# Kernel tuning notes

Hardware: AMD Instinct MI355X
Metric: run time of the kernel (lower is better)

The kernel has to match this reference:

```python
import jax, jax.numpy as jnp
import numpy as np

IGNORE_INDEX = 255
BOUNDARY_WEIGHT = 2.0


def setup_inputs() -> dict:
    key = jax.random.key(0)
    k1, k2 = jax.random.split(key)
    inputs = jax.random.normal(k1, (8, 21, 512, 512), dtype=jnp.float32)
    targets = jax.random.randint(k2, (8, 512, 512), 0, 21, dtype=jnp.int64)
    return {"inputs": inputs, "targets": targets}


def _boundary_map(targets):
    # Faithful to the original loops: for each interior (i, j), take the 3x3
    # patch over ALL batches; compute max-min over the ROW axis (dim=1) per
    # column; if ANY entry (across batch and the 3 columns) differs, mark
    # (i, j) as boundary for ALL batch elements.
    t = targets
    # row-wise (vertical) 3-tap max/min over rows i-1, i, i+1 -> (B, H-2, W)
    rmax = jnp.maximum(jnp.maximum(t[:, :-2, :], t[:, 1:-1, :]), t[:, 2:, :])
    rmin = jnp.minimum(jnp.minimum(t[:, :-2, :], t[:, 1:-1, :]), t[:, 2:, :])
    diff = (rmax - rmin) > 0  # (B, H-2, W)
    # any over the 3 patch columns j-1, j, j+1 -> (B, H-2, W-2)
    cany = diff[:, :, :-2] | diff[:, :, 1:-1] | diff[:, :, 2:]
    # any over batch (the original `.any()` reduces over everything)
    bmap = jnp.any(cany, axis=0)  # (H-2, W-2)
    boundary = jnp.zeros(t.shape, dtype=jnp.float32)
    boundary = boundary.at[:, 1:-1, 1:-1].set(
        jnp.broadcast_to(bmap.astype(jnp.float32), (t.shape[0],) + bmap.shape)
    )
    return boundary


def reference(inputs, targets):
    # per-pixel cross entropy with ignore_index (reduction='none' -> 0 at ignored)
    logp = jax.nn.log_softmax(inputs, axis=1)  # (B, C, H, W)
    valid = targets != IGNORE_INDEX
    safe_t = jnp.where(valid, targets, 0)
    ce = -jnp.take_along_axis(logp, safe_t[:, None, :, :], axis=1)[:, 0]  # (B,H,W)
    ce = jnp.where(valid, ce, 0.0)
    boundary = _boundary_map(targets)
    weighted = ce * (1.0 + BOUNDARY_WEIGHT * boundary)
    return weighted.mean()
```

## Files before the change

kernel.cpp:

```cpp
#include <hip/hip_runtime.h>

#define BATCH 8
#define NCLS 21
#define H 512
#define W 512
#define IGNORE_INDEX 255
#define HW (H * W)
#define NPIX (BATCH * HW)
#define NBLK 2048

typedef float vfloat4 __attribute__((ext_vector_type(4)));

__global__ __launch_bounds__(256)
void fused_kernel(const float* __restrict__ x, const int* __restrict__ t,
                  float* __restrict__ partial) {
    int tid = blockIdx.x * blockDim.x + threadIdx.x;
    int idx4 = tid << 2;
    int b = idx4 >> 18;
    int hw = idx4 & (HW - 1);
    int h = hw >> 9;
    int w = hw & (W - 1);

    unsigned bd0 = 0, bd1 = 0, bd2 = 0, bd3 = 0;
    if (h > 0 && h < H - 1) {
        int offL = (w == 0) ? 0 : -1;
        int offR = (w == W - 4) ? 3 : 4;
        #pragma unroll 1
        for (int bb = 0; bb < BATCH; ++bb) {
            const int* rm = t + bb * HW + h * W + w;
            const int* ra = rm - W;
            const int* rz = rm + W;
            int4 a4 = *(const int4*)ra;
            int4 m4 = *(const int4*)rm;
            int4 z4 = *(const int4*)rz;
            int aL = ra[offL], mL = rm[offL], zL = rz[offL];
            int aR = ra[offR], mR = rm[offR], zR = rz[offR];
            unsigned cdL = (unsigned)((aL != mL) | (mL != zL));
            unsigned cd0 = (unsigned)((a4.x != m4.x) | (m4.x != z4.x));
            unsigned cd1 = (unsigned)((a4.y != m4.y) | (m4.y != z4.y));
            unsigned cd2 = (unsigned)((a4.z != m4.z) | (m4.z != z4.z));
            unsigned cd3 = (unsigned)((a4.w != m4.w) | (m4.w != z4.w));
            unsigned cdR = (unsigned)((aR != mR) | (mR != zR));
            bd0 |= cdL | cd0 | cd1;
            bd1 |= cd0 | cd1 | cd2;
            bd2 |= cd1 | cd2 | cd3;
            bd3 |= cd2 | cd3 | cdR;
            if (bd0 & bd1 & bd2 & bd3) break;
        }
        if (w == 0) bd0 = 0;
        if (w == W - 4) bd3 = 0;
    }

    int4 tg = *(const int4*)(t + idx4);
    bool va0 = (tg.x != IGNORE_INDEX), va1 = (tg.y != IGNORE_INDEX);
    bool va2 = (tg.z != IGNORE_INDEX), va3 = (tg.w != IGNORE_INDEX);
    int st0 = va0 ? tg.x : 0, st1 = va1 ? tg.y : 0;
    int st2 = va2 ? tg.z : 0, st3 = va3 ? tg.w : 0;

    const float* p = x + (size_t)b * NCLS * HW + hw;
    float s0 = 0.f, s1 = 0.f, s2 = 0.f, s3 = 0.f;
    float xt0 = 0.f, xt1 = 0.f, xt2 = 0.f, xt3 = 0.f;
    #pragma unroll
    for (int c = 0; c < NCLS; ++c) {
        vfloat4 q = *(const vfloat4*)(p + (size_t)c * HW);
        s0 += __expf(q.x); if (c == st0) xt0 = q.x;
        s1 += __expf(q.y); if (c == st1) xt1 = q.y;
        s2 += __expf(q.z); if (c == st2) xt2 = q.z;
        s3 += __expf(q.w); if (c == st3) xt3 = q.w;
    }

    float ce0 = va0 ? (__logf(s0) - xt0) : 0.f;
    float ce1 = va1 ? (__logf(s1) - xt1) : 0.f;
    float ce2 = va2 ? (__logf(s2) - xt2) : 0.f;
    float ce3 = va3 ? (__logf(s3) - xt3) : 0.f;

    float local = ce0 * (1.f + 2.f * (float)bd0) + ce1 * (1.f + 2.f * (float)bd1) +
                  ce2 * (1.f + 2.f * (float)bd2) + ce3 * (1.f + 2.f * (float)bd3);

    #pragma unroll
    for (int off = 32; off > 0; off >>= 1)
        local += __shfl_down(local, off, 64);

    __shared__ float smem[4];
    int lane = threadIdx.x & 63;
    int wave = threadIdx.x >> 6;
    if (lane == 0) smem[wave] = local;
    __syncthreads();
    if (threadIdx.x == 0)
        partial[blockIdx.x] = smem[0] + smem[1] + smem[2] + smem[3];
}

__global__ void reduce_kernel(const float* __restrict__ partial,
                              float* __restrict__ out) {
    float s = 0.0f;
    for (int i = threadIdx.x; i < NBLK; i += 256) s += partial[i];
    #pragma unroll
    for (int off = 32; off > 0; off >>= 1)
        s += __shfl_down(s, off, 64);
    __shared__ float smem[4];
    int lane = threadIdx.x & 63;
    int wave = threadIdx.x >> 6;
    if (lane == 0) smem[wave] = s;
    __syncthreads();
    if (threadIdx.x == 0)
        out[0] = (smem[0] + smem[1] + smem[2] + smem[3]) * (1.0f / (float)NPIX);
}

extern "C" void kernel_launch(void* const* d_in, const int* in_sizes, int n_in,
                              void* d_out, int out_size, void* d_ws, size_t ws_size,
                              hipStream_t stream) {
    const float* x = (const float*)d_in[0];
    const int* t = (const int*)d_in[1];
    float* out = (float*)d_out;
    float* partial = (float*)d_ws;

    fused_kernel<<<NBLK, 256, 0, stream>>>(x, t, partial);
    reduce_kernel<<<1, 256, 0, stream>>>(partial, out);
}
```

Baseline: 248.9 us.

## Process two rows per thread with nontemporal prefetched logit loads

Each thread now handles 8 pixels, 4 columns in each of two rows two apart, so the grid is halved. Logit loads use nontemporal hints and are software-prefetched one class ahead. The boundary computation is moved into a helper that returns a bitmask. The intent is more memory-level parallelism per thread and less cache pollution from the streamed logits, at the cost of more registers per thread and fewer waves in flight.

```diff
diff --git a/kernel.cpp b/kernel.cpp
--- a/kernel.cpp
+++ b/kernel.cpp
@@ -7,21 +7,13 @@
 #define IGNORE_INDEX 255
 #define HW (H * W)
 #define NPIX (BATCH * HW)
-#define NBLK 2048
+#define NBLK 1024
 
 typedef float vfloat4 __attribute__((ext_vector_type(4)));
 
-__global__ __launch_bounds__(256)
-void fused_kernel(const float* __restrict__ x, const int* __restrict__ t,
-                  float* __restrict__ partial) {
-    int tid = blockIdx.x * blockDim.x + threadIdx.x;
-    int idx4 = tid << 2;
-    int b = idx4 >> 18;
-    int hw = idx4 & (HW - 1);
-    int h = hw >> 9;
-    int w = hw & (W - 1);
-
-    unsigned bd0 = 0, bd1 = 0, bd2 = 0, bd3 = 0;
+__device__ __forceinline__ unsigned boundary4(const int* __restrict__ t,
+                                              int h, int w) {
+    unsigned r = 0;
     if (h > 0 && h < H - 1) {
         int offL = (w == 0) ? 0 : -1;
         int offR = (w == W - 4) ? 3 : 4;
@@ -41,41 +33,81 @@
             unsigned cd2 = (unsigned)((a4.z != m4.z) | (m4.z != z4.z));
             unsigned cd3 = (unsigned)((a4.w != m4.w) | (m4.w != z4.w));
             unsigned cdR = (unsigned)((aR != mR) | (mR != zR));
-            bd0 |= cdL | cd0 | cd1;
-            bd1 |= cd0 | cd1 | cd2;
-            bd2 |= cd1 | cd2 | cd3;
-            bd3 |= cd2 | cd3 | cdR;
-            if (bd0 & bd1 & bd2 & bd3) break;
+            r |= (cdL | cd0 | cd1) | ((cd0 | cd1 | cd2) << 1) |
+                 ((cd1 | cd2 | cd3) << 2) | ((cd2 | cd3 | cdR) << 3);
+            if (r == 0xFu) break;
         }
-        if (w == 0) bd0 = 0;
-        if (w == W - 4) bd3 = 0;
+        if (w == 0) r &= ~1u;
+        if (w == W - 4) r &= ~8u;
+    }
+    return r;
+}
+
+__global__ __launch_bounds__(256)
+void fused_kernel(const float* __restrict__ x, const int* __restrict__ t,
+                  float* __restrict__ partial) {
+    int blk = blockIdx.x;
+    int b = blk >> 7;
+    int hq = blk & 127;
+    int i = threadIdx.x;
+    int h0 = (hq << 2) + (i >> 7);
+    int w = (i & 127) << 2;
+
+    int hw0 = (h0 << 9) + w;
+    int hw1 = hw0 + 2 * W;
+
+    unsigned bdA = boundary4(t, h0, w);
+    unsigned bdB = boundary4(t, h0 + 2, w);
+    int4 tgA = *(const int4*)(t + b * HW + hw0);
+    int4 tgB = *(const int4*)(t + b * HW + hw1);
+
+    bool vA0 = tgA.x != IGNORE_INDEX, vA1 = tgA.y != IGNORE_INDEX;
+    bool vA2 = tgA.z != IGNORE_INDEX, vA3 = tgA.w != IGNORE_INDEX;
+    bool vB0 = tgB.x != IGNORE_INDEX, vB1 = tgB.y != IGNORE_INDEX;
+    bool vB2 = tgB.z != IGNORE_INDEX, vB3 = tgB.w != IGNORE_INDEX;
+    int sA0 = vA0 ? tgA.x : 0, sA1 = vA1 ? tgA.y : 0;
+    int sA2 = vA2 ? tgA.z : 0, sA3 = vA3 ? tgA.w : 0;
+    int sB0 = vB0 ? tgB.x : 0, sB1 = vB1 ? tgB.y : 0;
+    int sB2 = vB2 ? tgB.z : 0, sB3 = vB3 ? tgB.w : 0;
+
+    const float* p0 = x + (size_t)b * NCLS * HW + hw0;
+    const float* p1 = x + (size_t)b * NCLS * HW + hw1;
+
+    vfloat4 a0 = __builtin_nontemporal_load((const vfloat4*)p0);
+    vfloat4 a1 = __builtin_nontemporal_load((const vfloat4*)p1);
+
+    float eA0 = 0.f, eA1 = 0.f, eA2 = 0.f, eA3 = 0.f;
+    float eB0 = 0.f, eB1 = 0.f, eB2 = 0.f, eB3 = 0.f;
+    float xA0 = 0.f, xA1 = 0.f, xA2 = 0.f, xA3 = 0.f;
+    float xB0 = 0.f, xB1 = 0.f, xB2 = 0.f, xB3 = 0.f;
+
+    #pragma unroll
+    for (int c = 0; c < NCLS; ++c) {
+        vfloat4 n0, n1;
+        if (c + 1 < NCLS) {
+            n0 = __builtin_nontemporal_load((const vfloat4*)(p0 + (size_t)(c + 1) * HW));
+            n1 = __builtin_nontemporal_load((const vfloat4*)(p1 + (size_t)(c + 1) * HW));
+        }
+        eA0 += __expf(a0.x); if (c == sA0) xA0 = a0.x;
+        eA1 += __expf(a0.y); if (c == sA1) xA1 = a0.y;
+        eA2 += __expf(a0.z); if (c == sA2) xA2 = a0.z;
+        eA3 += __expf(a0.w); if (c == sA3) xA3 = a0.w;
+        eB0 += __expf(a1.x); if (c == sB0) xB0 = a1.x;
+        eB1 += __expf(a1.y); if (c == sB1) xB1 = a1.y;
+        eB2 += __expf(a1.z); if (c == sB2) xB2 = a1.z;
+        eB3 += __expf(a1.w); if (c == sB3) xB3 = a1.w;
+        a0 = n0; a1 = n1;
     }
 
-    int4 tg = *(const int4*)(t + idx4);
-    bool va0 = (tg.x != IGNORE_INDEX), va1 = (tg.y != IGNORE_INDEX);
-    bool va2 = (tg.z != IGNORE_INDEX), va3 = (tg.w != IGNORE_INDEX);
-    int st0 = va0 ? tg.x : 0, st1 = va1 ? tg.y : 0;
-    int st2 = va2 ? tg.z : 0, st3 = va3 ? tg.w : 0;
-
-    const float* p = x + (size_t)b * NCLS * HW + hw;
-    float s0 = 0.f, s1 = 0.f, s2 = 0.f, s3 = 0.f;
-    float xt0 = 0.f, xt1 = 0.f, xt2 = 0.f, xt3 = 0.f;
-    #pragma unroll
-    for (int c = 0; c < NCLS; ++c) {
-        vfloat4 q = *(const vfloat4*)(p + (size_t)c * HW);
-        s0 += __expf(q.x); if (c == st0) xt0 = q.x;
-        s1 += __expf(q.y); if (c == st1) xt1 = q.y;
-        s2 += __expf(q.z); if (c == st2) xt2 = q.z;
-        s3 += __expf(q.w); if (c == st3) xt3 = q.w;
-    }
-
-    float ce0 = va0 ? (__logf(s0) - xt0) : 0.f;
-    float ce1 = va1 ? (__logf(s1) - xt1) : 0.f;
-    float ce2 = va2 ? (__logf(s2) - xt2) : 0.f;
-    float ce3 = va3 ? (__logf(s3) - xt3) : 0.f;
-
-    float local = ce0 * (1.f + 2.f * (float)bd0) + ce1 * (1.f + 2.f * (float)bd1) +
-                  ce2 * (1.f + 2.f * (float)bd2) + ce3 * (1.f + 2.f * (float)bd3);
+    float local =
+        (vA0 ? (__logf(eA0) - xA0) : 0.f) * (1.f + 2.f * (float)(bdA & 1u)) +
+        (vA1 ? (__logf(eA1) - xA1) : 0.f) * (1.f + 2.f * (float)((bdA >> 1) & 1u)) +
+        (vA2 ? (__logf(eA2) - xA2) : 0.f) * (1.f + 2.f * (float)((bdA >> 2) & 1u)) +
+        (vA3 ? (__logf(eA3) - xA3) : 0.f) * (1.f + 2.f * (float)((bdA >> 3) & 1u)) +
+        (vB0 ? (__logf(eB0) - xB0) : 0.f) * (1.f + 2.f * (float)(bdB & 1u)) +
+        (vB1 ? (__logf(eB1) - xB1) : 0.f) * (1.f + 2.f * (float)((bdB >> 1) & 1u)) +
+        (vB2 ? (__logf(eB2) - xB2) : 0.f) * (1.f + 2.f * (float)((bdB >> 2) & 1u)) +
+        (vB3 ? (__logf(eB3) - xB3) : 0.f) * (1.f + 2.f * (float)((bdB >> 3) & 1u));
 
     #pragma unroll
     for (int off = 32; off > 0; off >>= 1)
```

After: 236.0 us. 1.05x faster.
